# Kernel optimization log

Hardware: AMD Instinct MI355X
Metric: run time of the kernel (lower is better)

Reference implementation:

```python
import jax, jax.numpy as jnp
import numpy as np

DIM = 128

def _complex_linear_params(key, dim, scale=0.05):
    k1, k2, k3, k4 = jax.random.split(key, 4)
    Wr = jax.random.normal(k1, (dim, dim), jnp.float32) * scale
    Wi = jax.random.normal(k2, (dim, dim), jnp.float32) * scale
    br = jax.random.normal(k3, (dim,), jnp.float32) * scale
    bi = jax.random.normal(k4, (dim,), jnp.float32) * scale
    return Wr, Wi, br, bi

def setup_inputs() -> dict:
    key = jax.random.key(0)
    ks = jax.random.split(key, 8)
    B, C, Ht, Wt = 8, DIM, 64, 64
    Hs, Ws = 32, 32
    inp = {
        'target_r': jax.random.normal(ks[0], (B, C, Ht, Wt), jnp.float32),
        'target_i': jax.random.normal(ks[1], (B, C, Ht, Wt), jnp.float32),
        'source_r': jax.random.normal(ks[2], (B, C, Hs, Ws), jnp.float32),
        'source_i': jax.random.normal(ks[3], (B, C, Hs, Ws), jnp.float32),
    }
    for name, k in zip(('q', 'k', 'v'), ks[4:7]):
        Wr, Wi, br, bi = _complex_linear_params(k, DIM)
        inp[f'W{name}_r'], inp[f'W{name}_i'] = Wr, Wi
        inp[f'b{name}_r'], inp[f'b{name}_i'] = br, bi
    inp['gamma'] = jnp.float32(0.1)
    return inp

def reference(target_r, target_i, source_r, source_i,
              Wq_r, Wq_i, bq_r, bq_i,
              Wk_r, Wk_i, bk_r, bk_i,
              Wv_r, Wv_i, bv_r, bv_i, gamma):
    B, C, Ht, Wt = target_r.shape
    _, _, Hs, Ws = source_r.shape
    Nt, Ns = Ht * Wt, Hs * Ws
    scale = jnp.float32(C ** 0.5)
    # complex tensors [B, N, C]
    t = (target_r + 1j * target_i).reshape(B, C, Nt).transpose(0, 2, 1)
    s = (source_r + 1j * source_i).reshape(B, C, Ns).transpose(0, 2, 1)
    Wq = Wq_r + 1j * Wq_i; Wk = Wk_r + 1j * Wk_i; Wv = Wv_r + 1j * Wv_i
    Q = jnp.einsum('bnc,dc->bnd', t, Wq) + (bq_r + 1j * bq_i)
    K = jnp.einsum('bmc,dc->bmd', s, Wk) + (bk_r + 1j * bk_i)
    V = jnp.einsum('bmc,dc->bmd', s, Wv) + (bv_r + 1j * bv_i)
    # complex QK^H, keep only real part for softmax
    attn = jnp.einsum('bnd,bmd->bnm', Q, jnp.conj(K))  # [B, Nt, Ns] complex
    w = jax.nn.softmax(attn.real / scale, axis=-1)      # real weights
    out = jnp.einsum('bnm,bmd->bnd', w.astype(V.dtype), V)  # complex [B, Nt, C]
    out = out.transpose(0, 2, 1).reshape(B, C, Ht, Wt)
    return gamma * out
```

## Files before the change

### kernel.cpp

```cpp
#include <hip/hip_runtime.h>
#include <hip/hip_bf16.h>

#define NB 8
#define NC 128
#define NT 4096
#define NS 1024

typedef short bf16x8 __attribute__((ext_vector_type(8)));
typedef float f32x4  __attribute__((ext_vector_type(4)));

#define MFMA16(a, b, c) __builtin_amdgcn_mfma_f32_16x16x32_bf16(a, b, c, 0, 0, 0)

__device__ __forceinline__ short f2b(float x) {
    __hip_bfloat16 h = __float2bfloat16(x);
    return *reinterpret_cast<short*>(&h);
}

__device__ __forceinline__ void gl_lds16(const void* g, void* l) {
    __builtin_amdgcn_global_load_lds(
        (const __attribute__((address_space(1))) unsigned int*)g,
        (__attribute__((address_space(3))) unsigned int*)l, 16, 0, 0);
}

__global__ __launch_bounds__(256) void pack_w_kernel(
    const float* __restrict__ Wqr, const float* __restrict__ Wqi,
    const float* __restrict__ Wkr, const float* __restrict__ Wki,
    const float* __restrict__ Wvr, const float* __restrict__ Wvi,
    __hip_bfloat16* __restrict__ WqT, __hip_bfloat16* __restrict__ WkT,
    __hip_bfloat16* __restrict__ WvT)
{
    const int idx = blockIdx.x * 256 + threadIdx.x;
    const float *Wr, *Wi; __hip_bfloat16* dst; int base;
    if (idx < 65536)       { Wr = Wqr; Wi = Wqi; dst = WqT; base = idx; }
    else if (idx < 131072) { Wr = Wkr; Wi = Wki; dst = WkT; base = idx - 65536; }
    else                   { Wr = Wvr; Wi = Wvi; dst = WvT; base = idx - 131072; }
    const int dp = base >> 8, k = base & 255;
    const int d  = dp & 127;
    float v;
    if (dp < 128) v = (k < 128) ? Wr[d * 128 + k] : -Wi[d * 128 + k - 128];
    else          v = (k < 128) ? Wi[d * 128 + k] :  Wr[d * 128 + k - 128];
    dst[base] = __float2bfloat16(v);
}

__global__ __launch_bounds__(256) void projKV_kernel(
    const float* __restrict__ Xr, const float* __restrict__ Xi,
    const __hip_bfloat16* __restrict__ WkT, const __hip_bfloat16* __restrict__ WvT,
    const float* __restrict__ bkr, const float* __restrict__ bki,
    const float* __restrict__ bvr,
    __hip_bfloat16* __restrict__ Kh, __hip_bfloat16* __restrict__ VrT)
{
    __shared__ __align__(16) char smem[27136];
    const int b   = blockIdx.x & 7;
    const int n0  = (blockIdx.x >> 3) * 32;
    const int tid = threadIdx.x;

    for (int i = tid; i < 32 * 64; i += 256) {
        const int cp = i >> 5, n = i & 31, c = cp * 2;
        const size_t rb = (size_t)(b * NC + c) * NS + n0 + n;
        const unsigned pr = (unsigned short)f2b(Xr[rb]) |
                            ((unsigned)(unsigned short)f2b(Xr[rb + NS]) << 16);
        const unsigned pi = (unsigned short)f2b(Xi[rb]) |
                            ((unsigned)(unsigned short)f2b(Xi[rb + NS]) << 16);
        *(unsigned*)(smem + n * 528 + c * 2)         = pr;
        *(unsigned*)(smem + n * 528 + (128 + c) * 2) = pi;
    }
    __syncthreads();

    const int w = tid >> 6, l15 = tid & 15, q = (tid & 63) >> 4;
    const int r0 = (w & 1) * 16;
    const int g  = w >> 1;

    const char* wp[12];
    #pragma unroll
    for (int jj = 0; jj < 12; ++jj) {
        const int j = g * 12 + jj;
        wp[jj] = (j < 16)
            ? (const char*)WkT + (size_t)(j * 16 + l15) * 512 + q * 16
            : (const char*)WvT + (size_t)((j - 16) * 16 + l15) * 512 + q * 16;
    }

    f32x4 acc[12];
    #pragma unroll
    for (int jj = 0; jj < 12; ++jj) { acc[jj][0]=0.f; acc[jj][1]=0.f; acc[jj][2]=0.f; acc[jj][3]=0.f; }

    #pragma unroll
    for (int t = 0; t < 8; ++t) {
        const bf16x8 af = *(const bf16x8*)(smem + (r0 + l15) * 528 + (t * 32 + q * 8) * 2);
        #pragma unroll
        for (int jj = 0; jj < 12; ++jj) {
            const bf16x8 bf = *(const bf16x8*)(wp[jj] + t * 64);
            acc[jj] = MFMA16(af, bf, acc[jj]);
        }
    }

    #pragma unroll
    for (int jj = 0; jj < 12; ++jj) {
        const int j = g * 12 + jj;
        if (j < 16) {
            const int col = j * 16 + l15;
            const float bv = (col < 128) ? bkr[col] : bki[col - 128];
            #pragma unroll
            for (int r = 0; r < 4; ++r) {
                const int n = n0 + r0 + q * 4 + r;
                Kh[((size_t)(b * NS + n) << 8) + col] = __float2bfloat16(acc[jj][r] + bv);
            }
        } else {
            const int d = (j - 16) * 16 + l15;
            #pragma unroll
            for (int r = 0; r < 4; ++r)
                *(__hip_bfloat16*)(smem + 16896 + d * 80 + (r0 + q * 4 + r) * 2) =
                    __float2bfloat16(acc[jj][r] + bvr[d]);
        }
    }
    __syncthreads();
    for (int i = tid; i < 128 * 4; i += 256) {
        const int d = i >> 2, seg = i & 3;
        const int4 v = *(const int4*)(smem + 16896 + d * 80 + seg * 16);
        *(int4*)((char*)VrT + ((size_t)(b * NC + d) * NS + n0) * 2 + seg * 16) = v;
    }
}

__global__ __launch_bounds__(256, 2) void attn_mfma_kernel(
    const float* __restrict__ tr_g, const float* __restrict__ ti_g,
    const __hip_bfloat16* __restrict__ WqT,
    const float* __restrict__ bqr, const float* __restrict__ bqi,
    const __hip_bfloat16* __restrict__ Kh, const __hip_bfloat16* __restrict__ VrT,
    const float* __restrict__ gamma_p, float* __restrict__ out)
{
    __shared__ __align__(16) char smem[71680];
    char* As  = smem;
    char* kb0 = smem + 33792;
    char* kb1 = smem + 50176;
    char* ps  = smem + 66560;

    const int b    = blockIdx.x & 7;
    const int n0   = (blockIdx.x >> 3) * 64;
    const int tid  = threadIdx.x;
    const int w    = tid >> 6, lane = tid & 63, l15 = tid & 15, q = (tid & 63) >> 4;
    const int row0 = w * 16;
    char* psw = ps + w * 1280;

    for (int i = tid; i < 64 * 64; i += 256) {
        const int cp = i >> 6, n = i & 63, c = cp * 2;
        const size_t rb = (size_t)(b * NC + c) * NT + n0 + n;
        const unsigned pr = (unsigned short)f2b(tr_g[rb]) |
                            ((unsigned)(unsigned short)f2b(tr_g[rb + NT]) << 16);
        const unsigned pi = (unsigned short)f2b(ti_g[rb]) |
                            ((unsigned)(unsigned short)f2b(ti_g[rb + NT]) << 16);
        *(unsigned*)(As + n * 528 + c * 2)         = pr;
        *(unsigned*)(As + n * 528 + (128 + c) * 2) = pi;
    }

    const char* Kbase = (const char*)Kh + ((size_t)(b * NS) << 9);
    #pragma unroll
    for (int i = 0; i < 4; ++i) {
        const int ml = w * 8 + i * 2 + (lane >> 5);
        const int so = ml * 512 + ((((lane & 31) ^ (ml & 7))) << 4);
        gl_lds16(Kbase + so, kb0 + (w * 4 + i) * 1024);
    }
    __syncthreads();

    {
        f32x4 qacc[16];
        #pragma unroll
        for (int j = 0; j < 16; ++j) { qacc[j][0]=0.f; qacc[j][1]=0.f; qacc[j][2]=0.f; qacc[j][3]=0.f; }
        #pragma unroll
        for (int t = 0; t < 8; ++t) {
            const bf16x8 af = *(const bf16x8*)(As + (row0 + l15) * 528 + (t * 32 + q * 8) * 2);
            #pragma unroll
            for (int j = 0; j < 16; ++j) {
                const int col = j * 16 + l15;
                const bf16x8 bf = *(const bf16x8*)((const char*)WqT + col * 512 + (t * 32 + q * 8) * 2);
                qacc[j] = MFMA16(af, bf, qacc[j]);
            }
        }
        __syncthreads();
        const float inv_s = 0.08838834764831845f;
        #pragma unroll
        for (int j = 0; j < 16; ++j) {
            const int col  = j * 16 + l15;
            const float bv = (col < 128) ? bqr[col] : bqi[col - 128];
            #pragma unroll
            for (int r = 0; r < 4; ++r) {
                const int row = row0 + q * 4 + r;
                *(__hip_bfloat16*)(As + row * 528 + col * 2) =
                    __float2bfloat16((qacc[j][r] + bv) * inv_s);
            }
        }
    }
    __syncthreads();

    bf16x8 qf[8];
    #pragma unroll
    for (int t = 0; t < 8; ++t)
        qf[t] = *(const bf16x8*)(As + (row0 + l15) * 528 + (t * 32 + q * 8) * 2);

    f32x4 oacc[8];
    #pragma unroll
    for (int j = 0; j < 8; ++j) { oacc[j][0]=0.f; oacc[j][1]=0.f; oacc[j][2]=0.f; oacc[j][3]=0.f; }
    float m_run[4] = {-1e30f, -1e30f, -1e30f, -1e30f};
    float l_run[4] = {0.f, 0.f, 0.f, 0.f};

    const char* vp[8];
    #pragma unroll
    for (int j = 0; j < 8; ++j)
        vp[j] = (const char*)VrT + (size_t)(b * NC + j * 16 + l15) * (NS * 2) + q * 16;

    const int e3 = l15 & 7;
    const int qx = q ^ (e3 & 3);
    const int eh = e3 >> 2;

    char* kbc = kb0;
    char* kbn = kb1;

    #pragma unroll 1
    for (int ch = 0; ch < 32; ++ch) {
        bf16x8 vfr[8];
        #pragma unroll
        for (int j = 0; j < 8; ++j) { vfr[j] = *(const bf16x8*)vp[j]; vp[j] += 64; }

        const size_t sb = (size_t)((ch < 31 ? ch + 1 : 31) * 32) * 512;
        #pragma unroll
        for (int i = 0; i < 4; ++i) {
            const int ml = w * 8 + i * 2 + (lane >> 5);
            const int so = ml * 512 + ((((lane & 31) ^ (ml & 7))) << 4);
            gl_lds16(Kbase + sb + so, kbn + (w * 4 + i) * 1024);
        }

        f32x4 s0v, s1v;
        s0v[0]=0.f; s0v[1]=0.f; s0v[2]=0.f; s0v[3]=0.f;
        s1v[0]=0.f; s1v[1]=0.f; s1v[2]=0.f; s1v[3]=0.f;
        #pragma unroll
        for (int t = 0; t < 8; ++t) {
            const int tb = ((t ^ eh) << 6) + (qx << 4);
            const bf16x8 k0 = *(const bf16x8*)(kbc + l15 * 512 + tb);
            s0v = MFMA16(qf[t], k0, s0v);
            const bf16x8 k1 = *(const bf16x8*)(kbc + (16 + l15) * 512 + tb);
            s1v = MFMA16(qf[t], k1, s1v);
        }

        float alpha_r[4];
        #pragma unroll
        for (int r = 0; r < 4; ++r) {
            float mx = fmaxf(s0v[r], s1v[r]);
            #pragma unroll
            for (int off = 8; off >= 1; off >>= 1)
                mx = fmaxf(mx, __shfl_xor(mx, off, 16));
            const float mn = fmaxf(m_run[r], mx);
            const float a  = __expf(m_run[r] - mn);
            m_run[r] = mn; alpha_r[r] = a;
            const float p0 = __expf(s0v[r] - mn);
            const float p1 = __expf(s1v[r] - mn);
            s0v[r] = p0; s1v[r] = p1;
            float sum = p0 + p1;
            #pragma unroll
            for (int off = 8; off >= 1; off >>= 1)
                sum += __shfl_xor(sum, off, 16);
            l_run[r] = l_run[r] * a + sum;
        }

        #pragma unroll
        for (int r = 0; r < 4; ++r) {
            *(__hip_bfloat16*)(psw + (q * 4 + r) * 80 + l15 * 2) =
                __float2bfloat16(s0v[r]);
            *(__hip_bfloat16*)(psw + (q * 4 + r) * 80 + (16 + l15) * 2) =
                __float2bfloat16(s1v[r]);
        }

        #pragma unroll
        for (int j = 0; j < 8; ++j) {
            #pragma unroll
            for (int r = 0; r < 4; ++r) oacc[j][r] *= alpha_r[r];
        }

        const bf16x8 pf = *(const bf16x8*)(psw + l15 * 80 + q * 16);
        #pragma unroll
        for (int j = 0; j < 8; ++j)
            oacc[j] = MFMA16(pf, vfr[j], oacc[j]);

        __syncthreads();
        char* tsw = kbc; kbc = kbn; kbn = tsw;
    }

    float* Of = (float*)smem;
    const float g = gamma_p[0];
    #pragma unroll
    for (int r = 0; r < 4; ++r) {
        const float inv_l = g / fmaxf(l_run[r], 1e-30f);
        const int m = row0 + q * 4 + r;
        #pragma unroll
        for (int j = 0; j < 8; ++j)
            Of[(j * 16 + l15) * 65 + m] = oacc[j][r] * inv_l;
    }
    __syncthreads();
    float* ob = out + (size_t)b * NC * NT + n0;
    for (int i = tid; i < 128 * 64; i += 256) {
        const int d = i >> 6, m = i & 63;
        ob[(size_t)d * NT + m] = Of[d * 65 + m];
    }
}

extern "C" void kernel_launch(void* const* d_in, const int* in_sizes, int n_in,
                              void* d_out, int out_size, void* d_ws, size_t ws_size,
                              hipStream_t stream)
{
    const float* target_r = (const float*)d_in[0];
    const float* target_i = (const float*)d_in[1];
    const float* source_r = (const float*)d_in[2];
    const float* source_i = (const float*)d_in[3];
    const float* Wq_r = (const float*)d_in[4];
    const float* Wq_i = (const float*)d_in[5];
    const float* bq_r = (const float*)d_in[6];
    const float* bq_i = (const float*)d_in[7];
    const float* Wk_r = (const float*)d_in[8];
    const float* Wk_i = (const float*)d_in[9];
    const float* bk_r = (const float*)d_in[10];
    const float* bk_i = (const float*)d_in[11];
    const float* Wv_r = (const float*)d_in[12];
    const float* Wv_i = (const float*)d_in[13];
    const float* bv_r = (const float*)d_in[14];
    const float* bv_i = (const float*)d_in[15];
    const float* gamma = (const float*)d_in[16];

    char* ws = (char*)d_ws;
    __hip_bfloat16* Kh  = (__hip_bfloat16*)(ws);
    __hip_bfloat16* VrT = (__hip_bfloat16*)(ws + 4194304);
    __hip_bfloat16* WqT = (__hip_bfloat16*)(ws + 6291456);
    __hip_bfloat16* WkT = (__hip_bfloat16*)(ws + 6422528);
    __hip_bfloat16* WvT = (__hip_bfloat16*)(ws + 6553600);

    pack_w_kernel<<<640, 256, 0, stream>>>(Wq_r, Wq_i, Wk_r, Wk_i, Wv_r, Wv_i,
                                           WqT, WkT, WvT);

    projKV_kernel<<<NB * (NS / 32), 256, 0, stream>>>(
        source_r, source_i, WkT, WvT, bk_r, bk_i, bv_r, Kh, VrT);

    attn_mfma_kernel<<<NB * (NT / 64), 256, 0, stream>>>(
        target_r, target_i, WqT, bq_r, bq_i, Kh, VrT, gamma, (float*)d_out);
}
```

Baseline: 228.6 us.

## Stage V through LDS with triple-buffered K/V prefetch two chunks ahead

V tiles now reach LDS through async global-to-LDS loads with an XOR swizzle, packed next to the K tile, instead of being read straight from global memory into registers each iteration. A three-buffer ring prefetches two chunks ahead, and the trailing per-iteration __syncthreads is replaced by a vmcnt wait plus barrier at the top of the loop. The goal is to hide global latency for both K and V and cut register pressure from the V fragments. In exchange LDS use grows to about 77 KB, which may limit occupancy, and the hand-written vmcnt count must match the number of loads issued.

```diff
diff --git a/kernel.cpp b/kernel.cpp
--- a/kernel.cpp
+++ b/kernel.cpp
@@ -120,6 +120,25 @@
     }
 }
 
+__device__ __forceinline__ void stage_chunk(const char* Kbase, const char* Vbase,
+                                            char* buf, int ch, int w, int lane)
+{
+    const char* ks = Kbase + (size_t)ch * 16384;
+    #pragma unroll
+    for (int i = 0; i < 4; ++i) {
+        const int ml = w * 8 + i * 2 + (lane >> 5);
+        const int so = ml * 512 + (((lane & 31) ^ (ml & 7)) << 4);
+        gl_lds16(ks + so, buf + (w * 4 + i) * 1024);
+    }
+    const char* vsrc = Vbase + (size_t)ch * 64;
+    #pragma unroll
+    for (int i = 0; i < 2; ++i) {
+        const int d  = (w + i * 4) * 16 + (lane >> 2);
+        const int so = d * 2048 + (((lane & 3) ^ ((lane >> 2) & 3)) << 4);
+        gl_lds16(vsrc + so, buf + 16384 + (w + i * 4) * 1024);
+    }
+}
+
 __global__ __launch_bounds__(256, 2) void attn_mfma_kernel(
     const float* __restrict__ tr_g, const float* __restrict__ ti_g,
     const __hip_bfloat16* __restrict__ WqT,
@@ -127,11 +146,9 @@
     const __hip_bfloat16* __restrict__ Kh, const __hip_bfloat16* __restrict__ VrT,
     const float* __restrict__ gamma_p, float* __restrict__ out)
 {
-    __shared__ __align__(16) char smem[71680];
-    char* As  = smem;
-    char* kb0 = smem + 33792;
-    char* kb1 = smem + 50176;
-    char* ps  = smem + 66560;
+    __shared__ __align__(16) char smem[78848];
+    char* As = smem;
+    char* ps = smem + 73728;
 
     const int b    = blockIdx.x & 7;
     const int n0   = (blockIdx.x >> 3) * 64;
@@ -150,16 +167,9 @@
         *(unsigned*)(As + n * 528 + c * 2)         = pr;
         *(unsigned*)(As + n * 528 + (128 + c) * 2) = pi;
     }
-
-    const char* Kbase = (const char*)Kh + ((size_t)(b * NS) << 9);
-    #pragma unroll
-    for (int i = 0; i < 4; ++i) {
-        const int ml = w * 8 + i * 2 + (lane >> 5);
-        const int so = ml * 512 + ((((lane & 31) ^ (ml & 7))) << 4);
-        gl_lds16(Kbase + so, kb0 + (w * 4 + i) * 1024);
-    }
-    __syncthreads();
-
+    __syncthreads();
+
+    bf16x8 qf[8];
     {
         f32x4 qacc[16];
         #pragma unroll
@@ -174,7 +184,6 @@
                 qacc[j] = MFMA16(af, bf, qacc[j]);
             }
         }
-        __syncthreads();
         const float inv_s = 0.08838834764831845f;
         #pragma unroll
         for (int j = 0; j < 16; ++j) {
@@ -187,13 +196,20 @@
                     __float2bfloat16((qacc[j][r] + bv) * inv_s);
             }
         }
-    }
-    __syncthreads();
-
-    bf16x8 qf[8];
-    #pragma unroll
-    for (int t = 0; t < 8; ++t)
-        qf[t] = *(const bf16x8*)(As + (row0 + l15) * 528 + (t * 32 + q * 8) * 2);
+        #pragma unroll
+        for (int t = 0; t < 8; ++t)
+            qf[t] = *(const bf16x8*)(As + (row0 + l15) * 528 + (t * 32 + q * 8) * 2);
+    }
+    __syncthreads();
+
+    const char* Kbase = (const char*)Kh + ((size_t)(b * NS) << 9);
+    const char* Vbase = (const char*)VrT + (size_t)b * NC * NS * 2;
+    char* bA = smem;
+    char* bB = smem + 24576;
+    char* bC = smem + 49152;
+
+    stage_chunk(Kbase, Vbase, bA, 0, w, lane);
+    stage_chunk(Kbase, Vbase, bB, 1, w, lane);
 
     f32x4 oacc[8];
     #pragma unroll
@@ -201,31 +217,18 @@
     float m_run[4] = {-1e30f, -1e30f, -1e30f, -1e30f};
     float l_run[4] = {0.f, 0.f, 0.f, 0.f};
 
-    const char* vp[8];
-    #pragma unroll
-    for (int j = 0; j < 8; ++j)
-        vp[j] = (const char*)VrT + (size_t)(b * NC + j * 16 + l15) * (NS * 2) + q * 16;
-
-    const int e3 = l15 & 7;
-    const int qx = q ^ (e3 & 3);
-    const int eh = e3 >> 2;
-
-    char* kbc = kb0;
-    char* kbn = kb1;
+    const int e3   = l15 & 7;
+    const int qx   = q ^ (e3 & 3);
+    const int eh   = e3 >> 2;
+    const int vswz = (q ^ (l15 & 3)) << 4;
 
     #pragma unroll 1
     for (int ch = 0; ch < 32; ++ch) {
-        bf16x8 vfr[8];
-        #pragma unroll
-        for (int j = 0; j < 8; ++j) { vfr[j] = *(const bf16x8*)vp[j]; vp[j] += 64; }
-
-        const size_t sb = (size_t)((ch < 31 ? ch + 1 : 31) * 32) * 512;
-        #pragma unroll
-        for (int i = 0; i < 4; ++i) {
-            const int ml = w * 8 + i * 2 + (lane >> 5);
-            const int so = ml * 512 + ((((lane & 31) ^ (ml & 7))) << 4);
-            gl_lds16(Kbase + sb + so, kbn + (w * 4 + i) * 1024);
-        }
+        asm volatile("s_waitcnt vmcnt(6)" ::: "memory");
+        __builtin_amdgcn_s_barrier();
+
+        const int sch = (ch + 2 < 32) ? ch + 2 : 31;
+        stage_chunk(Kbase, Vbase, bC, sch, w, lane);
 
         f32x4 s0v, s1v;
         s0v[0]=0.f; s0v[1]=0.f; s0v[2]=0.f; s0v[3]=0.f;
@@ -233,9 +236,9 @@
         #pragma unroll
         for (int t = 0; t < 8; ++t) {
             const int tb = ((t ^ eh) << 6) + (qx << 4);
-            const bf16x8 k0 = *(const bf16x8*)(kbc + l15 * 512 + tb);
+            const bf16x8 k0 = *(const bf16x8*)(bA + l15 * 512 + tb);
             s0v = MFMA16(qf[t], k0, s0v);
-            const bf16x8 k1 = *(const bf16x8*)(kbc + (16 + l15) * 512 + tb);
+            const bf16x8 k1 = *(const bf16x8*)(bA + (16 + l15) * 512 + tb);
             s1v = MFMA16(qf[t], k1, s1v);
         }
 
@@ -275,13 +278,15 @@
 
         const bf16x8 pf = *(const bf16x8*)(psw + l15 * 80 + q * 16);
         #pragma unroll
-        for (int j = 0; j < 8; ++j)
-            oacc[j] = MFMA16(pf, vfr[j], oacc[j]);
-
-        __syncthreads();
-        char* tsw = kbc; kbc = kbn; kbn = tsw;
-    }
-
+        for (int j = 0; j < 8; ++j) {
+            const bf16x8 vf = *(const bf16x8*)(bA + 16384 + (j * 16 + l15) * 64 + vswz);
+            oacc[j] = MFMA16(pf, vf, oacc[j]);
+        }
+
+        char* t0 = bA; bA = bB; bB = bC; bC = t0;
+    }
+
+    __syncthreads();
     float* Of = (float*)smem;
     const float g = gamma_p[0];
     #pragma unroll
```

Result: faster. 222.1 us (-2.8%).
